# Kernel tuning notes

Hardware: AMD Instinct MI355X
Metric: run time of the kernel (lower is better)

The kernel has to match this reference:

```python
import jax, jax.numpy as jnp
import numpy as np

T, E, H, V, K = 1024, 300, 512, 100000, 12
START, STOP = 10, 11


def setup_inputs() -> dict:
    key = jax.random.key(0)
    ks = jax.random.split(key, 12)
    s = 0.05
    sentence = jax.random.randint(ks[0], (T,), 0, V, dtype=jnp.int32)
    tags = jax.random.randint(ks[1], (T,), 0, START, dtype=jnp.int32)  # real tags only
    word_embeds = jax.random.normal(ks[2], (V, E), jnp.float32) * 0.1

    def lstm_p(k):
        k1, k2 = jax.random.split(k)
        return (jax.random.normal(k1, (4 * H, E), jnp.float32) * s,
                jax.random.normal(k2, (4 * H, H), jnp.float32) * s,
                jnp.zeros(4 * H, jnp.float32), jnp.zeros(4 * H, jnp.float32))

    Wih_f, Whh_f, bih_f, bhh_f = lstm_p(ks[3])
    Wih_b, Whh_b, bih_b, bhh_b = lstm_p(ks[4])
    D = 2 * H
    attn_W = jax.random.normal(ks[5], (D, D), jnp.float32) * s
    attn_b = jnp.zeros(D, jnp.float32)
    h2h1_W = jax.random.normal(ks[6], (D, 2 * D), jnp.float32) * s
    h2h1_b = jnp.zeros(D, jnp.float32)
    tag_W = jax.random.normal(ks[7], (K, D), jnp.float32) * s
    tag_b = jnp.zeros(K, jnp.float32)
    transitions = jax.random.normal(ks[8], (K, K), jnp.float32) * 0.01
    transitions = transitions.at[START, :].set(-10000.0).at[:, STOP].set(-10000.0)
    return dict(sentence=sentence, tags=tags, word_embeds=word_embeds,
                Wih_f=Wih_f, Whh_f=Whh_f, bih_f=bih_f, bhh_f=bhh_f,
                Wih_b=Wih_b, Whh_b=Whh_b, bih_b=bih_b, bhh_b=bhh_b,
                attn_W=attn_W, attn_b=attn_b, h2h1_W=h2h1_W, h2h1_b=h2h1_b,
                tag_W=tag_W, tag_b=tag_b, transitions=transitions)


def _lstm_pass(x, Wih, Whh, bih, bhh):
    # x: [T, E] -> hs: [T, H]   (PyTorch LSTM gate order i,f,g,o)
    xg = x @ Wih.T + bih  # [T, 4H] precomputed input contribution

    def step(carry, g_in):
        h, c = carry
        g = g_in + h @ Whh.T + bhh
        i, f, gg, o = jnp.split(g, 4)
        i = jax.nn.sigmoid(i); f = jax.nn.sigmoid(f)
        gg = jnp.tanh(gg); o = jax.nn.sigmoid(o)
        c = f * c + i * gg
        h = o * jnp.tanh(c)
        return (h, c), h

    init = (jnp.zeros(H, x.dtype), jnp.zeros(H, x.dtype))
    _, hs = jax.lax.scan(step, init, xg)
    return hs


def reference(sentence, tags, word_embeds, Wih_f, Whh_f, bih_f, bhh_f,
              Wih_b, Whh_b, bih_b, bhh_b, attn_W, attn_b,
              h2h1_W, h2h1_b, tag_W, tag_b, transitions):
    x = word_embeds[sentence]                       # [T, E]  (dropout is eval no-op)
    h_fwd = _lstm_pass(x, Wih_f, Whh_f, bih_f, bhh_f)
    h_bwd = _lstm_pass(x[::-1], Wih_b, Whh_b, bih_b, bhh_b)[::-1]
    enc = jnp.concatenate([h_fwd, h_bwd], axis=-1)  # [T, 2H]

    # Attn 'general': energy(t, i) = enc[t] . (W enc[i] + b); vectorized per-timestep loop
    proj = enc @ attn_W.T + attn_b                  # [T, 2H]
    scores = enc @ proj.T                           # [T, T]
    w = jax.nn.softmax(scores, axis=-1)
    ctx = w @ enc                                   # [T, 2H]

    h1 = jnp.tanh(jnp.concatenate([enc, ctx], axis=-1) @ h2h1_W.T + h2h1_b)  # [T, 2H]
    feats = h1 @ tag_W.T + tag_b                    # [T, K]

    # CRF forward algorithm (log partition); transitions[to, from]
    alpha0 = jnp.full((K,), -10000.0, feats.dtype).at[START].set(0.0)

    def crf_step(alpha, feat):
        a = jax.nn.logsumexp(alpha[None, :] + transitions, axis=1) + feat
        return a, None

    alpha, _ = jax.lax.scan(crf_step, alpha0, feats)
    logZ = jax.nn.logsumexp(alpha + transitions[STOP])

    # gold path score (_score_sentence)
    pad_start = jnp.concatenate([jnp.array([START], tags.dtype), tags])
    pad_stop = jnp.concatenate([tags, jnp.array([STOP], tags.dtype)])
    gold = transitions[pad_stop, pad_start].sum() + feats[jnp.arange(T), tags].sum()

    return logZ - gold  # CRF negative log-likelihood for this sentence
```

## Files before the change

kernel.cpp:

```cpp
#include <hip/hip_runtime.h>
#include <hip/hip_fp16.h>

#define T_LEN 1024
#define E_DIM 300
#define H_DIM 512
#define D_DIM 1024
#define K_TAGS 12
#define G4 2048

typedef __attribute__((ext_vector_type(8))) short short8x;
typedef __attribute__((ext_vector_type(4))) float f32x4;

static __device__ __forceinline__ float frcp(float x){ return __builtin_amdgcn_rcpf(x); }
static __device__ __forceinline__ float sigm(float x){ return frcp(1.f + __expf(-x)); }
static __device__ __forceinline__ float ftanh(float x){
  const float e = __expf(2.f * fabsf(x));
  const float t = 1.f - 2.f * frcp(e + 1.f);
  return copysignf(t, x);
}
static __device__ __forceinline__ unsigned short f2b(float f){
  unsigned u = __float_as_uint(f);
  return (unsigned short)((u + 0x7fffu + ((u >> 16) & 1u)) >> 16);
}
static __device__ __forceinline__ uint4 pack8(const float* s){
  uint4 o;
  o.x = (unsigned)f2b(s[0]) | ((unsigned)f2b(s[1]) << 16);
  o.y = (unsigned)f2b(s[2]) | ((unsigned)f2b(s[3]) << 16);
  o.z = (unsigned)f2b(s[4]) | ((unsigned)f2b(s[5]) << 16);
  o.w = (unsigned)f2b(s[6]) | ((unsigned)f2b(s[7]) << 16);
  return o;
}
static __device__ __forceinline__ uint4 pack8u(const unsigned short* s){
  uint4 o;
  o.x = (unsigned)s[0] | ((unsigned)s[1] << 16);
  o.y = (unsigned)s[2] | ((unsigned)s[3] << 16);
  o.z = (unsigned)s[4] | ((unsigned)s[5] << 16);
  o.w = (unsigned)s[6] | ((unsigned)s[7] << 16);
  return o;
}

__global__ void k_gather(const int* __restrict__ sent, const float* __restrict__ we,
                         unsigned short* __restrict__ xh){
  int idx = blockIdx.x*256 + threadIdx.x;
  if (idx < T_LEN*E_DIM){
    int t = idx / E_DIM, e = idx - t*E_DIM;
    xh[idx] = f2b(we[(size_t)sent[t]*E_DIM + e]);
  }
}

__global__ __launch_bounds__(256) void k_cast(const float* __restrict__ src,
                                              unsigned short* __restrict__ dst,
                                              int n4){
  int i = blockIdx.x*256 + threadIdx.x;
  if (i < n4){
    const float4 v = *reinterpret_cast<const float4*>(src + (size_t)i*4);
    ushort2 a, b;
    a.x = f2b(v.x); a.y = f2b(v.y); b.x = f2b(v.z); b.y = f2b(v.w);
    *reinterpret_cast<ushort2*>(dst + (size_t)i*4)     = a;
    *reinterpret_cast<ushort2*>(dst + (size_t)i*4 + 2) = b;
  }
}

__global__ void k_init(unsigned* __restrict__ hbuf){
  int i = blockIdx.x*256 + threadIdx.x;
  if (i < 2048) hbuf[i] = 0u;
}

__global__ __launch_bounds__(256) void k_gemm_mfma(
    const unsigned short* __restrict__ Ah, int lda, int arev,
    const unsigned short* __restrict__ Bh, int ldb,
    const float* __restrict__ bias, int act,
    void* __restrict__ Cp, int ldc, int cbf16, int M, int N, int K)
{
  __shared__ __align__(16) unsigned short As[64*40];
  __shared__ __align__(16) unsigned short Bs[64*40];
  const int tid = threadIdx.x;
  const int bm = blockIdx.y*64, bn = blockIdx.x*64;
  const int r  = tid >> 2, c8 = (tid & 3) * 8;
  const int wave = tid >> 6, lane = tid & 63;
  const int wm = (wave >> 1) * 32, wn = (wave & 1) * 32;
  const int col = lane & 15, quad = lane >> 4;

  const int am = arev ? (M-1-(bm+r)) : (bm+r);
  const unsigned short* arow = Ah + (size_t)am*lda;
  const unsigned short* brow = Bh + (size_t)(bn+r)*ldb;

  uint4* aw = (uint4*)(As + r*40 + c8);
  uint4* bw = (uint4*)(Bs + r*40 + c8);

  f32x4 acc[2][2];
  #pragma unroll
  for (int i=0;i<2;i++)
    #pragma unroll
    for (int j=0;j<2;j++) acc[i][j] = (f32x4){0.f,0.f,0.f,0.f};

  for (int k0 = 0; k0 < K; k0 += 32){
    uint4 avv, bvv;
    if (k0 + 32 <= K){
      avv = *(const uint4*)(arow + k0 + c8);
      bvv = *(const uint4*)(brow + k0 + c8);
    } else {
      unsigned short ta[8], tb[8];
      #pragma unroll
      for (int i=0;i<8;i++){
        const int kk = k0 + c8 + i;
        ta[i] = (kk < K) ? arow[kk] : (unsigned short)0;
        tb[i] = (kk < K) ? brow[kk] : (unsigned short)0;
      }
      avv = pack8u(ta); bvv = pack8u(tb);
    }
    if (k0) __syncthreads();
    *aw = avv; *bw = bvv;
    __syncthreads();
    const short8x a0 = *(const short8x*)(As + (wm+col)*40    + quad*8);
    const short8x a1 = *(const short8x*)(As + (wm+16+col)*40 + quad*8);
    const short8x b0 = *(const short8x*)(Bs + (wn+col)*40    + quad*8);
    const short8x b1 = *(const short8x*)(Bs + (wn+16+col)*40 + quad*8);
    acc[0][0] = __builtin_amdgcn_mfma_f32_16x16x32_bf16(a0, b0, acc[0][0], 0, 0, 0);
    acc[0][1] = __builtin_amdgcn_mfma_f32_16x16x32_bf16(a0, b1, acc[0][1], 0, 0, 0);
    acc[1][0] = __builtin_amdgcn_mfma_f32_16x16x32_bf16(a1, b0, acc[1][0], 0, 0, 0);
    acc[1][1] = __builtin_amdgcn_mfma_f32_16x16x32_bf16(a1, b1, acc[1][1], 0, 0, 0);
  }

  #pragma unroll
  for (int mt=0;mt<2;mt++){
    #pragma unroll
    for (int nt=0;nt<2;nt++){
      const int cc = bn + wn + 16*nt + col;
      const float bs = bias ? bias[cc] : 0.f;
      #pragma unroll
      for (int i=0;i<4;i++){
        const int rr = bm + wm + 16*mt + quad*4 + i;
        float v = acc[mt][nt][i] + bs;
        if (act) v = ftanh(v);
        if (cbf16) ((unsigned short*)Cp)[(size_t)rr*ldc + cc] = f2b(v);
        else       ((float*)Cp)[(size_t)rr*ldc + cc] = v;
      }
    }
  }
}

__global__ __launch_bounds__(256, 1) void k_lstm(
    const float* __restrict__ Whh_f, const float* __restrict__ Whh_b,
    const float* __restrict__ bih_f, const float* __restrict__ bhh_f,
    const float* __restrict__ bih_b, const float* __restrict__ bhh_b,
    const float* __restrict__ xg_f, const float* __restrict__ xg_b,
    unsigned* __restrict__ hbuf, float* __restrict__ enc)
{
  const int dir = blockIdx.x >> 5;
  const int w   = blockIdx.x & 31;
  const int tid = threadIdx.x;
  const int wave = tid >> 6, lane = tid & 63;
  const int col = lane & 15, quad = lane >> 4;

  const float* Whh = dir ? Whh_b : Whh_f;
  const float* xg  = dir ? xg_b  : xg_f;

  const int rowA = wave*H_DIM + w*16 + col;
  short8x w_frag[16];
  #pragma unroll
  for (int s=0;s<16;s++){
    const float* bp = Whh + (size_t)rowA*H_DIM + s*32 + quad*8;
    uint4 u = pack8(bp);
    w_frag[s] = *reinterpret_cast<short8x*>(&u);
  }

  float bias_r = 0.f, xg_cur = 0.f, c_reg = 0.f;
  int row2 = 0;
  if (tid < 64){
    row2 = (tid >> 4)*H_DIM + w*16 + (tid & 15);
    bias_r = dir ? (bih_b[row2] + bhh_b[row2]) : (bih_f[row2] + bhh_f[row2]);
    xg_cur = xg[row2];
  }

  __shared__ __align__(16) unsigned short lds_hb[512];
  __shared__ __align__(16) float raw[64];

  unsigned* hb = hbuf + dir*1024;

  for (int t = 1; t <= T_LEN; ++t){
    {
      unsigned* s0 = hb + ((t-1)&1)*512 + tid;
      const unsigned want = (unsigned)(t-1);
      unsigned v0 = __hip_atomic_load(s0,     __ATOMIC_RELAXED, __HIP_MEMORY_SCOPE_AGENT);
      unsigned v1 = __hip_atomic_load(s0+256, __ATOMIC_RELAXED, __HIP_MEMORY_SCOPE_AGENT);
      while (((v0 >> 16) != want) || ((v1 >> 16) != want)){
        v0 = __hip_atomic_load(s0,     __ATOMIC_RELAXED, __HIP_MEMORY_SCOPE_AGENT);
        v1 = __hip_atomic_load(s0+256, __ATOMIC_RELAXED, __HIP_MEMORY_SCOPE_AGENT);
      }
      lds_hb[tid]     = (unsigned short)(v0 & 0xffffu);
      lds_hb[tid+256] = (unsigned short)(v1 & 0xffffu);
    }
    __syncthreads();

    float xg_nxt = 0.f;
    if (tid < 64 && t < T_LEN) xg_nxt = xg[(size_t)t*G4 + row2];

    f32x4 a0 = (f32x4){0.f,0.f,0.f,0.f}, a1 = (f32x4){0.f,0.f,0.f,0.f};
    #pragma unroll
    for (int s=0;s<16;s+=2){
      const short8x b0 = *(const short8x*)(lds_hb + s*32     + quad*8);
      const short8x b1 = *(const short8x*)(lds_hb + (s+1)*32 + quad*8);
      a0 = __builtin_amdgcn_mfma_f32_16x16x32_bf16(w_frag[s],   b0, a0, 0, 0, 0);
      a1 = __builtin_amdgcn_mfma_f32_16x16x32_bf16(w_frag[s+1], b1, a1, 0, 0, 0);
    }
    if (col == 0){
      f32x4 asum = a0 + a1;
      *reinterpret_cast<f32x4*>(raw + wave*16 + quad*4) = asum;
    }
    __syncthreads();

    if (tid < 64){
      float v = raw[tid] + bias_r + xg_cur;
      const float va = ((tid >> 4) == 2) ? ftanh(v) : sigm(v);
      const int l2 = tid & 15;
      const float iv = __shfl(va, l2);
      const float fv = __shfl(va, l2 + 16);
      const float gg = __shfl(va, l2 + 32);
      const float ov = __shfl(va, l2 + 48);
      if (tid < 16){
        c_reg = fv*c_reg + iv*gg;
        const float hh = ov*ftanh(c_reg);
        const int hj = w*16 + tid;
        const unsigned hv = ((unsigned)t << 16) | (unsigned)f2b(hh);
        __hip_atomic_store(hb + (t&1)*512 + hj, hv,
                           __ATOMIC_RELAXED, __HIP_MEMORY_SCOPE_AGENT);
        const int tt = dir ? (T_LEN - t) : (t - 1);
        enc[(size_t)tt*D_DIM + dir*H_DIM + hj] = hh;
      }
      xg_cur = xg_nxt;
    }
    __syncthreads();
  }
}

__global__ __launch_bounds__(256) void k_softmax(float* __restrict__ S,
                                                 unsigned short* __restrict__ Sh){
  float* r = S + (size_t)blockIdx.x*1024;
  unsigned short* rh = Sh + (size_t)blockIdx.x*1024;
  const int tid = threadIdx.x;
  float v[4];
  #pragma unroll
  for (int i=0;i<4;i++) v[i] = r[tid + i*256];
  float m = fmaxf(fmaxf(v[0],v[1]), fmaxf(v[2],v[3]));
  #pragma unroll
  for (int off=32; off>=1; off>>=1) m = fmaxf(m, __shfl_xor(m, off));
  __shared__ float red[4], red2[4];
  const int wid = tid >> 6, lane = tid & 63;
  if (lane == 0) red[wid] = m;
  __syncthreads();
  m = fmaxf(fmaxf(red[0],red[1]), fmaxf(red[2],red[3]));
  float s = 0.f;
  #pragma unroll
  for (int i=0;i<4;i++){ v[i] = __expf(v[i]-m); s += v[i]; }
  #pragma unroll
  for (int off=32; off>=1; off>>=1) s += __shfl_xor(s, off);
  if (lane == 0) red2[wid] = s;
  __syncthreads();
  s = red2[0]+red2[1]+red2[2]+red2[3];
  const float inv = frcp(s);
  #pragma unroll
  for (int i=0;i<4;i++){
    const float o = v[i]*inv;
    r[tid + i*256]  = o;
    rh[tid + i*256] = f2b(o);
  }
}

__global__ void k_copy_enc(const float* __restrict__ enc,
                           unsigned short* __restrict__ cath){
  int idx = blockIdx.x*256 + threadIdx.x;
  if (idx < T_LEN*D_DIM){
    int t = idx >> 10, d = idx & 1023;
    cath[(size_t)t*2048 + d] = f2b(enc[idx]);
  }
}

__global__ __launch_bounds__(256) void k_castT(const float* __restrict__ src,
                                               unsigned short* __restrict__ dst){
  __shared__ float tile[32][33];
  const int bx = blockIdx.x*32, by = blockIdx.y*32;
  const int tx = threadIdx.x & 31, ty8 = threadIdx.x >> 5;
  #pragma unroll
  for (int i=ty8;i<32;i+=8) tile[i][tx] = src[(size_t)(by+i)*1024 + bx+tx];
  __syncthreads();
  #pragma unroll
  for (int i=ty8;i<32;i+=8) dst[(size_t)(bx+i)*1024 + by+tx] = f2b(tile[tx][i]);
}

__global__ __launch_bounds__(256) void k_feats(
    const float* __restrict__ h1, const float* __restrict__ tagW,
    const float* __restrict__ tagb, float* __restrict__ feats)
{
  const int t = blockIdx.x;
  const int wave = threadIdx.x >> 6, lane = threadIdx.x & 63;
  const float* hr = h1 + (size_t)t*D_DIM;
  float hv[16];
  #pragma unroll
  for (int i=0;i<16;i++) hv[i] = hr[lane + 64*i];
  #pragma unroll
  for (int j=0;j<3;j++){
    const int tag = wave*3 + j;
    const float* wr = tagW + (size_t)tag*D_DIM;
    float s = 0.f;
    #pragma unroll
    for (int i=0;i<16;i++) s += hv[i]*wr[lane + 64*i];
    #pragma unroll
    for (int off=32; off>=1; off>>=1) s += __shfl_xor(s, off);
    if (lane == 0) feats[(size_t)t*K_TAGS + tag] = s + tagb[tag];
  }
}

__global__ __launch_bounds__(64) void k_crf1(const float* __restrict__ feats,
                                             const float* __restrict__ trans,
                                             float* __restrict__ chunkM){
  const int c = blockIdx.x;
  const int r = threadIdx.x;
  __shared__ float sT[144];
  __shared__ float sF[16*12];
  for (int i=r; i<144; i+=64) sT[i] = trans[i];
  const int t0 = c*16;
  for (int i=r; i<192; i+=64) sF[i] = feats[(size_t)t0*K_TAGS + i];
  __syncthreads();
  if (r < 12){
    float m[12], nm[12];
    #pragma unroll
    for (int k=0;k<12;k++) m[k] = sT[k*12 + r] + sF[k];
    for (int s=1; s<16; ++s){
      #pragma unroll
      for (int i=0;i<12;i++){
        float v[12]; float mx = -1e30f;
        #pragma unroll
        for (int k=0;k<12;k++){ v[k] = sT[i*12+k] + m[k]; mx = fmaxf(mx, v[k]); }
        float ss = 0.f;
        #pragma unroll
        for (int k=0;k<12;k++) ss += __expf(v[k]-mx);
        nm[i] = sF[s*12+i] + mx + __logf(ss);
      }
      #pragma unroll
      for (int i=0;i<12;i++) m[i] = nm[i];
    }
    #pragma unroll
    for (int k=0;k<12;k++) chunkM[c*144 + k*12 + r] = m[k];
  }
}

__global__ __launch_bounds__(128) void k_crf2(const float* __restrict__ chunkM,
                                              const float* __restrict__ feats,
                                              const float* __restrict__ trans,
                                              const int* __restrict__ tags,
                                              float* __restrict__ out){
  const int tid = threadIdx.x, wave = tid >> 6, lane = tid & 63;
  __shared__ float sGold;
  float alpha = (lane == 10) ? 0.f : -10000.f;
  if (wave == 1){
    float g = 0.f;
    for (int i = lane; i <= T_LEN; i += 64){
      const int to = (i < T_LEN) ? tags[i]   : 11;
      const int fr = (i == 0)    ? 10        : tags[i-1];
      g += trans[to*K_TAGS + fr];
      if (i < T_LEN) g += feats[(size_t)i*K_TAGS + tags[i]];
    }
    #pragma unroll
    for (int off=32; off>=1; off>>=1) g += __shfl_xor(g, off);
    if (lane == 0) sGold = g;
  } else {
    float pf[12];
    #pragma unroll
    for (int k=0;k<12;k++) pf[k] = (lane < 12) ? chunkM[lane*12 + k] : 0.f;
    for (int c=0; c<64; ++c){
      float av[12];
      #pragma unroll
      for (int j=0;j<12;j++) av[j] = __shfl(alpha, j);
      float cur[12];
      #pragma unroll
      for (int k=0;k<12;k++) cur[k] = pf[k];
      if (c+1 < 64){
        #pragma unroll
        for (int k=0;k<12;k++)
          pf[k] = (lane < 12) ? chunkM[(c+1)*144 + lane*12 + k] : 0.f;
      }
      if (lane < 12){
        float v[12]; float mx = -1e30f;
        #pragma unroll
        for (int k=0;k<12;k++){ v[k] = cur[k] + av[k]; mx = fmaxf(mx, v[k]); }
        float ss = 0.f;
        #pragma unroll
        for (int k=0;k<12;k++) ss += __expf(v[k]-mx);
        alpha = mx + __logf(ss);
      }
    }
  }
  __syncthreads();
  if (wave == 0){
    float v = (lane < K_TAGS) ? (alpha + trans[11*K_TAGS + lane]) : -1e30f;
    float m = v;
    #pragma unroll
    for (int off=32; off>=1; off>>=1) m = fmaxf(m, __shfl_xor(m, off));
    float e = (lane < K_TAGS) ? __expf(v - m) : 0.f;
    #pragma unroll
    for (int off=32; off>=1; off>>=1) e += __shfl_xor(e, off);
    if (lane == 0) out[0] = (m + __logf(e)) - sGold;
  }
}

extern "C" void kernel_launch(void* const* d_in, const int* in_sizes, int n_in,
                              void* d_out, int out_size, void* d_ws, size_t ws_size,
                              hipStream_t stream)
{
  const int*   sentence = (const int*)d_in[0];
  const int*   tags     = (const int*)d_in[1];
  const float* we       = (const float*)d_in[2];
  const float* Wih_f    = (const float*)d_in[3];
  const float* Whh_f    = (const float*)d_in[4];
  const float* bih_f    = (const float*)d_in[5];
  const float* bhh_f    = (const float*)d_in[6];
  const float* Wih_b    = (const float*)d_in[7];
  const float* Whh_b    = (const float*)d_in[8];
  const float* bih_b    = (const float*)d_in[9];
  const float* bhh_b    = (const float*)d_in[10];
  const float* attn_W   = (const float*)d_in[11];
  const float* attn_b   = (const float*)d_in[12];
  const float* h2h1_W   = (const float*)d_in[13];
  const float* h2h1_b   = (const float*)d_in[14];
  const float* tag_W    = (const float*)d_in[15];
  const float* tag_b    = (const float*)d_in[16];
  const float* trans    = (const float*)d_in[17];
  float* out = (float*)d_out;

  float* ws = (float*)d_ws;
  float* R1 = ws;
  float* R2 = ws + 2097152;
  float* R3 = ws + 4194304;
  float* R4 = ws + 5242880;
  float* feats = ws + 6291456;
  unsigned* hbuf = (unsigned*)(ws + 6303744);

  float* xg_f = R1;
  float* xg_b = R2;
  float* enc  = R3;
  unsigned short* xh      = (unsigned short*)R4;
  unsigned short* Wih_fh  = (unsigned short*)R4 + 307200;
  unsigned short* Wih_bh  = (unsigned short*)R4 + 921600;
  unsigned short* cath    = (unsigned short*)R1;
  unsigned short* attn_Wh = (unsigned short*)(R1 + 1048576);
  unsigned short* h2h1_Wh = (unsigned short*)R2;
  float* scores = R2 + 1048576;
  unsigned short* encT    = (unsigned short*)R4;
  unsigned short* projh   = (unsigned short*)R4 + 1048576;
  unsigned short* scoresh = (unsigned short*)R3;
  float* h1     = R3;
  float* chunkM = R4;

  k_gather<<<dim3((T_LEN*E_DIM + 255)/256), dim3(256), 0, stream>>>(sentence, we, xh);
  k_init<<<dim3(8), dim3(256), 0, stream>>>(hbuf);
  k_cast<<<dim3(600),  dim3(256), 0, stream>>>(Wih_f, Wih_fh, 153600);
  k_cast<<<dim3(600),  dim3(256), 0, stream>>>(Wih_b, Wih_bh, 153600);
  k_gemm_mfma<<<dim3(32,16), dim3(256), 0, stream>>>(xh, E_DIM, 0,
      Wih_fh, E_DIM, nullptr, 0, xg_f, G4, 0, T_LEN, G4, E_DIM);
  k_gemm_mfma<<<dim3(32,16), dim3(256), 0, stream>>>(xh, E_DIM, 1,
      Wih_bh, E_DIM, nullptr, 0, xg_b, G4, 0, T_LEN, G4, E_DIM);
  k_lstm<<<dim3(64), dim3(256), 0, stream>>>(Whh_f, Whh_b, bih_f, bhh_f,
      bih_b, bhh_b, xg_f, xg_b, hbuf, enc);
  k_copy_enc<<<dim3(4096), dim3(256), 0, stream>>>(enc, cath);
  k_castT<<<dim3(32,32), dim3(256), 0, stream>>>(enc, encT);
  k_cast<<<dim3(1024), dim3(256), 0, stream>>>(attn_W, attn_Wh, 262144);
  k_cast<<<dim3(2048), dim3(256), 0, stream>>>(h2h1_W, h2h1_Wh, 524288);
  k_gemm_mfma<<<dim3(16,16), dim3(256), 0, stream>>>(cath, 2048, 0,
      attn_Wh, D_DIM, attn_b, 0, projh, D_DIM, 1, T_LEN, D_DIM, D_DIM);
  k_gemm_mfma<<<dim3(16,16), dim3(256), 0, stream>>>(cath, 2048, 0,
      projh, D_DIM, nullptr, 0, scores, T_LEN, 0, T_LEN, T_LEN, D_DIM);
  k_softmax<<<dim3(1024), dim3(256), 0, stream>>>(scores, scoresh);
  k_gemm_mfma<<<dim3(16,16), dim3(256), 0, stream>>>(scoresh, T_LEN, 0,
      encT, D_DIM, nullptr, 0, cath + 1024, 2048, 1, T_LEN, D_DIM, T_LEN);
  k_gemm_mfma<<<dim3(16,16), dim3(256), 0, stream>>>(cath, 2048, 0,
      h2h1_Wh, 2048, h2h1_b, 1, h1, D_DIM, 0, T_LEN, D_DIM, 2048);
  k_feats<<<dim3(1024), dim3(256), 0, stream>>>(h1, tag_W, tag_b, feats);
  k_crf1<<<dim3(64), dim3(64), 0, stream>>>(feats, trans, chunkM);
  k_crf2<<<dim3(1), dim3(128), 0, stream>>>(chunkM, feats, trans, tags, out);
}
```

Measured before the change: 1.790 ms.

## Fuse input-projection GEMM into LSTM kernel with per-block ready flags

After: 1.823 ms. No clear change (+1.9%).

```diff
diff --git a/kernel.cpp b/kernel.cpp
--- a/kernel.cpp
+++ b/kernel.cpp
@@ -61,13 +61,14 @@
   }
 }
 
-__global__ void k_init(unsigned* __restrict__ hbuf){
+__global__ void k_init(unsigned* __restrict__ hbuf, unsigned* __restrict__ rdy){
   int i = blockIdx.x*256 + threadIdx.x;
   if (i < 2048) hbuf[i] = 0u;
+  if (i < 32)   rdy[i]  = 0u;
 }
 
 __global__ __launch_bounds__(256) void k_gemm_mfma(
-    const unsigned short* __restrict__ Ah, int lda, int arev,
+    const unsigned short* __restrict__ Ah, int lda,
     const unsigned short* __restrict__ Bh, int ldb,
     const float* __restrict__ bias, int act,
     void* __restrict__ Cp, int ldc, int cbf16, int M, int N, int K)
@@ -81,8 +82,7 @@
   const int wm = (wave >> 1) * 32, wn = (wave & 1) * 32;
   const int col = lane & 15, quad = lane >> 4;
 
-  const int am = arev ? (M-1-(bm+r)) : (bm+r);
-  const unsigned short* arow = Ah + (size_t)am*lda;
+  const unsigned short* arow = Ah + (size_t)(bm+r)*lda;
   const unsigned short* brow = Bh + (size_t)(bn+r)*ldb;
 
   uint4* aw = (uint4*)(As + r*40 + c8);
@@ -140,21 +140,95 @@
   }
 }
 
-__global__ __launch_bounds__(256, 1) void k_lstm(
+__global__ __launch_bounds__(256, 1) void k_lstm_fused(
     const float* __restrict__ Whh_f, const float* __restrict__ Whh_b,
     const float* __restrict__ bih_f, const float* __restrict__ bhh_f,
     const float* __restrict__ bih_b, const float* __restrict__ bhh_b,
-    const float* __restrict__ xg_f, const float* __restrict__ xg_b,
-    unsigned* __restrict__ hbuf, float* __restrict__ enc)
+    float* __restrict__ xg_f, float* __restrict__ xg_b,
+    const unsigned short* __restrict__ xh,
+    const unsigned short* __restrict__ Wih_fh, const unsigned short* __restrict__ Wih_bh,
+    unsigned* __restrict__ hbuf, unsigned* __restrict__ xgReady,
+    float* __restrict__ enc)
 {
-  const int dir = blockIdx.x >> 5;
-  const int w   = blockIdx.x & 31;
+  __shared__ __align__(16) unsigned short As[64*40];
+  __shared__ __align__(16) unsigned short Bs[64*40];
+  __shared__ __align__(16) unsigned short lds_hb[512];
+  __shared__ __align__(16) float raw[64];
+
   const int tid = threadIdx.x;
   const int wave = tid >> 6, lane = tid & 63;
   const int col = lane & 15, quad = lane >> 4;
 
+  if (blockIdx.x >= 64){
+    const int pid = blockIdx.x - 64;
+    const int r  = tid >> 2, c8 = (tid & 3) * 8;
+    const int wm = (wave >> 1) * 32, wn = (wave & 1) * 32;
+    uint4* aw = (uint4*)(As + r*40 + c8);
+    uint4* bw = (uint4*)(Bs + r*40 + c8);
+
+    for (int j = pid; j < 1024; j += 192){
+      const int bm = j >> 6, rem = j & 63, pdir = rem >> 5, bn = rem & 31;
+      const unsigned short* Bh = pdir ? Wih_bh : Wih_fh;
+      float* C = pdir ? xg_b : xg_f;
+      const int am = pdir ? (1023 - (bm*64 + r)) : (bm*64 + r);
+      const unsigned short* arow = xh + (size_t)am*E_DIM;
+      const unsigned short* brow = Bh + (size_t)(bn*64 + r)*E_DIM;
+
+      f32x4 acc[2][2];
+      #pragma unroll
+      for (int i=0;i<2;i++)
+        #pragma unroll
+        for (int jj=0;jj<2;jj++) acc[i][jj] = (f32x4){0.f,0.f,0.f,0.f};
+
+      for (int k0 = 0; k0 < E_DIM; k0 += 32){
+        uint4 avv, bvv;
+        if (k0 + 32 <= E_DIM){
+          avv = *(const uint4*)(arow + k0 + c8);
+          bvv = *(const uint4*)(brow + k0 + c8);
+        } else {
+          unsigned short ta[8], tb[8];
+          #pragma unroll
+          for (int i=0;i<8;i++){
+            const int kk = k0 + c8 + i;
+            ta[i] = (kk < E_DIM) ? arow[kk] : (unsigned short)0;
+            tb[i] = (kk < E_DIM) ? brow[kk] : (unsigned short)0;
+          }
+          avv = pack8u(ta); bvv = pack8u(tb);
+        }
+        __syncthreads();
+        *aw = avv; *bw = bvv;
+        __syncthreads();
+        const short8x a0 = *(const short8x*)(As + (wm+col)*40    + quad*8);
+        const short8x a1 = *(const short8x*)(As + (wm+16+col)*40 + quad*8);
+        const short8x b0 = *(const short8x*)(Bs + (wn+col)*40    + quad*8);
+        const short8x b1 = *(const short8x*)(Bs + (wn+16+col)*40 + quad*8);
+        acc[0][0] = __builtin_amdgcn_mfma_f32_16x16x32_bf16(a0, b0, acc[0][0], 0, 0, 0);
+        acc[0][1] = __builtin_amdgcn_mfma_f32_16x16x32_bf16(a0, b1, acc[0][1], 0, 0, 0);
+        acc[1][0] = __builtin_amdgcn_mfma_f32_16x16x32_bf16(a1, b0, acc[1][0], 0, 0, 0);
+        acc[1][1] = __builtin_amdgcn_mfma_f32_16x16x32_bf16(a1, b1, acc[1][1], 0, 0, 0);
+      }
+      #pragma unroll
+      for (int mt=0;mt<2;mt++)
+        #pragma unroll
+        for (int nt=0;nt<2;nt++)
+          #pragma unroll
+          for (int i=0;i<4;i++)
+            C[(size_t)(bm*64 + wm + 16*mt + quad*4 + i)*G4 + (bn*64 + wn + 16*nt + col)]
+              = acc[mt][nt][i];
+      __syncthreads();
+      if (tid == 0)
+        __hip_atomic_fetch_add(&xgReady[pdir*16 + bm], 1u,
+                               __ATOMIC_RELEASE, __HIP_MEMORY_SCOPE_AGENT);
+    }
+    return;
+  }
+
+  const int dir = blockIdx.x >> 5;
+  const int w   = blockIdx.x & 31;
+
   const float* Whh = dir ? Whh_b : Whh_f;
   const float* xg  = dir ? xg_b  : xg_f;
+  unsigned* rdy = xgReady + dir*16;
 
   const int rowA = wave*H_DIM + w*16 + col;
   short8x w_frag[16];
@@ -166,15 +240,15 @@
   }
 
   float bias_r = 0.f, xg_cur = 0.f, c_reg = 0.f;
-  int row2 = 0;
+  int row2 = 0, readyBlk = 0;
   if (tid < 64){
     row2 = (tid >> 4)*H_DIM + w*16 + (tid & 15);
     bias_r = dir ? (bih_b[row2] + bhh_b[row2]) : (bih_f[row2] + bhh_f[row2]);
+    while (__hip_atomic_load(rdy, __ATOMIC_RELAXED, __HIP_MEMORY_SCOPE_AGENT) != 32u) {}
+    (void)__hip_atomic_load(rdy, __ATOMIC_ACQUIRE, __HIP_MEMORY_SCOPE_AGENT);
+    readyBlk = 1;
     xg_cur = xg[row2];
   }
-
-  __shared__ __align__(16) unsigned short lds_hb[512];
-  __shared__ __align__(16) float raw[64];
 
   unsigned* hb = hbuf + dir*1024;
 
@@ -194,7 +268,15 @@
     __syncthreads();
 
     float xg_nxt = 0.f;
-    if (tid < 64 && t < T_LEN) xg_nxt = xg[(size_t)t*G4 + row2];
+    if (tid < 64 && t < T_LEN){
+      const int nb = t >> 6;
+      if (nb >= readyBlk){
+        while (__hip_atomic_load(rdy + nb, __ATOMIC_RELAXED, __HIP_MEMORY_SCOPE_AGENT) != 32u) {}
+        (void)__hip_atomic_load(rdy + nb, __ATOMIC_ACQUIRE, __HIP_MEMORY_SCOPE_AGENT);
+        readyBlk = nb + 1;
+      }
+      xg_nxt = xg[(size_t)t*G4 + row2];
+    }
 
     f32x4 a0 = (f32x4){0.f,0.f,0.f,0.f}, a1 = (f32x4){0.f,0.f,0.f,0.f};
     #pragma unroll
@@ -267,25 +349,21 @@
   }
 }
 
-__global__ void k_copy_enc(const float* __restrict__ enc,
-                           unsigned short* __restrict__ cath){
-  int idx = blockIdx.x*256 + threadIdx.x;
-  if (idx < T_LEN*D_DIM){
-    int t = idx >> 10, d = idx & 1023;
-    cath[(size_t)t*2048 + d] = f2b(enc[idx]);
-  }
-}
-
-__global__ __launch_bounds__(256) void k_castT(const float* __restrict__ src,
-                                               unsigned short* __restrict__ dst){
+__global__ __launch_bounds__(256) void k_encprep(const float* __restrict__ src,
+                                                 unsigned short* __restrict__ cath,
+                                                 unsigned short* __restrict__ encT){
   __shared__ float tile[32][33];
   const int bx = blockIdx.x*32, by = blockIdx.y*32;
   const int tx = threadIdx.x & 31, ty8 = threadIdx.x >> 5;
   #pragma unroll
-  for (int i=ty8;i<32;i+=8) tile[i][tx] = src[(size_t)(by+i)*1024 + bx+tx];
+  for (int i=ty8;i<32;i+=8){
+    const float v = src[(size_t)(by+i)*1024 + bx+tx];
+    tile[i][tx] = v;
+    cath[(size_t)(by+i)*2048 + bx+tx] = f2b(v);
+  }
   __syncthreads();
   #pragma unroll
-  for (int i=ty8;i<32;i+=8) dst[(size_t)(bx+i)*1024 + by+tx] = f2b(tile[tx][i]);
+  for (int i=ty8;i<32;i+=8) encT[(size_t)(bx+i)*1024 + by+tx] = f2b(tile[tx][i]);
 }
 
 __global__ __launch_bounds__(256) void k_feats(
@@ -442,6 +520,7 @@
   unsigned short* xh      = (unsigned short*)R4;
   unsigned short* Wih_fh  = (unsigned short*)R4 + 307200;
   unsigned short* Wih_bh  = (unsigned short*)R4 + 921600;
+  unsigned* xgReady = (unsigned*)feats;
   unsigned short* cath    = (unsigned short*)R1;
   unsigned short* attn_Wh = (unsigned short*)(R1 + 1048576);
   unsigned short* h2h1_Wh = (unsigned short*)R2;
@@ -453,27 +532,22 @@
   float* chunkM = R4;
 
   k_gather<<<dim3((T_LEN*E_DIM + 255)/256), dim3(256), 0, stream>>>(sentence, we, xh);
-  k_init<<<dim3(8), dim3(256), 0, stream>>>(hbuf);
+  k_init<<<dim3(8), dim3(256), 0, stream>>>(hbuf, xgReady);
   k_cast<<<dim3(600),  dim3(256), 0, stream>>>(Wih_f, Wih_fh, 153600);
   k_cast<<<dim3(600),  dim3(256), 0, stream>>>(Wih_b, Wih_bh, 153600);
-  k_gemm_mfma<<<dim3(32,16), dim3(256), 0, stream>>>(xh, E_DIM, 0,
-      Wih_fh, E_DIM, nullptr, 0, xg_f, G4, 0, T_LEN, G4, E_DIM);
-  k_gemm_mfma<<<dim3(32,16), dim3(256), 0, stream>>>(xh, E_DIM, 1,
-      Wih_bh, E_DIM, nullptr, 0, xg_b, G4, 0, T_LEN, G4, E_DIM);
-  k_lstm<<<dim3(64), dim3(256), 0, stream>>>(Whh_f, Whh_b, bih_f, bhh_f,
-      bih_b, bhh_b, xg_f, xg_b, hbuf, enc);
-  k_copy_enc<<<dim3(4096), dim3(256), 0, stream>>>(enc, cath);
-  k_castT<<<dim3(32,32), dim3(256), 0, stream>>>(enc, encT);
+  k_lstm_fused<<<dim3(256), dim3(256), 0, stream>>>(Whh_f, Whh_b, bih_f, bhh_f,
+      bih_b, bhh_b, xg_f, xg_b, xh, Wih_fh, Wih_bh, hbuf, xgReady, enc);
+  k_encprep<<<dim3(32,32), dim3(256), 0, stream>>>(enc, cath, encT);
   k_cast<<<dim3(1024), dim3(256), 0, stream>>>(attn_W, attn_Wh, 262144);
   k_cast<<<dim3(2048), dim3(256), 0, stream>>>(h2h1_W, h2h1_Wh, 524288);
-  k_gemm_mfma<<<dim3(16,16), dim3(256), 0, stream>>>(cath, 2048, 0,
+  k_gemm_mfma<<<dim3(16,16), dim3(256), 0, stream>>>(cath, 2048,
       attn_Wh, D_DIM, attn_b, 0, projh, D_DIM, 1, T_LEN, D_DIM, D_DIM);
-  k_gemm_mfma<<<dim3(16,16), dim3(256), 0, stream>>>(cath, 2048, 0,
+  k_gemm_mfma<<<dim3(16,16), dim3(256), 0, stream>>>(cath, 2048,
       projh, D_DIM, nullptr, 0, scores, T_LEN, 0, T_LEN, T_LEN, D_DIM);
   k_softmax<<<dim3(1024), dim3(256), 0, stream>>>(scores, scoresh);
-  k_gemm_mfma<<<dim3(16,16), dim3(256), 0, stream>>>(scoresh, T_LEN, 0,
+  k_gemm_mfma<<<dim3(16,16), dim3(256), 0, stream>>>(scoresh, T_LEN,
       encT, D_DIM, nullptr, 0, cath + 1024, 2048, 1, T_LEN, D_DIM, T_LEN);
-  k_gemm_mfma<<<dim3(16,16), dim3(256), 0, stream>>>(cath, 2048, 0,
+  k_gemm_mfma<<<dim3(16,16), dim3(256), 0, stream>>>(cath, 2048,
       h2h1_Wh, 2048, h2h1_b, 1, h1, D_DIM, 0, T_LEN, D_DIM, 2048);
   k_feats<<<dim3(1024), dim3(256), 0, stream>>>(h1, tag_W, tag_b, feats);
   k_crf1<<<dim3(64), dim3(64), 0, stream>>>(feats, trans, chunkM);
```
